# Optimization experiments

Measured on AMD Instinct MI355X. Metric: run time of the kernel, lower is better.

The kernel has to match this reference:

```python
import jax, jax.numpy as jnp
import numpy as np

N_NODES = 100000
N_EDGES = 1_600_000


def setup_inputs() -> dict:
    key = jax.random.key(0)
    ks = jax.random.split(key, 18)
    glorot = lambda k, fi, fo: jax.random.normal(k, (fi, fo), jnp.float32) * np.sqrt(2.0 / (fi + fo))
    inp = {
        "x": jax.random.normal(ks[0], (N_NODES, 5), jnp.float32),
        "edge_index": jax.random.randint(ks[1], (2, N_EDGES), 0, N_NODES, jnp.int64 if jax.config.jax_enable_x64 else jnp.int32),
        "W1": glorot(ks[2], 5, 32),  "b1": jnp.zeros((32,), jnp.float32),
        "W2": glorot(ks[3], 32, 32), "b2": jnp.zeros((32,), jnp.float32),
        "W3": glorot(ks[4], 32, 32), "b3": jnp.zeros((32,), jnp.float32),
        "Wd": glorot(ks[5], 32, 1),  "bd": jnp.zeros((1,), jnp.float32),
        "Wa": glorot(ks[6], 32, 1),  "ba": jnp.zeros((1,), jnp.float32),
        "Wt": glorot(ks[7], 32, 2),  "bt": jnp.zeros((2,), jnp.float32),
        "Wact": glorot(ks[8], 32, 9), "bact": jnp.zeros((9,), jnp.float32),
    }
    return inp


def _gcn_layer(x, row, col, norm, W, b):
    # GCNConv(add_self_loops=False): out[col] += norm * (x @ W)[row], then + bias
    h = x @ W                                  # [N, F_out]
    msg = h[row] * norm[:, None]               # [E, F_out]
    return jax.ops.segment_sum(msg, col, num_segments=N_NODES) + b


def reference(x, edge_index, W1, b1, W2, b2, W3, b3, Wd, bd, Wa, ba, Wt, bt, Wact, bact):
    row, col = edge_index[0], edge_index[1]
    # symmetric gcn normalization: deg over targets (unit edge weights)
    deg = jax.ops.segment_sum(jnp.ones((row.shape[0],), x.dtype), col, num_segments=N_NODES)
    dis = jnp.where(deg > 0, jax.lax.rsqrt(jnp.maximum(deg, 1.0)), 0.0)
    norm = dis[row] * dis[col]                 # [E]

    h = jax.nn.relu(_gcn_layer(x, row, col, norm, W1, b1))   # dropout = identity (eval)
    h = jax.nn.relu(_gcn_layer(h, row, col, norm, W2, b2))
    h = jax.nn.relu(_gcn_layer(h, row, col, norm, W3, b3))

    distance_scores = (h @ Wd + bd)[:, 0]      # [N]
    attention_scores = (h @ Wa + ba)[:, 0]     # [N]
    target_idx = jnp.argmax(attention_scores)
    h_t = h[target_idx]                        # [32]
    target_location_score = h_t @ Wt + bt      # [2]
    action_logits = h_t @ Wact + bact          # [9]
    return distance_scores, attention_scores, target_location_score, action_logits
```

## Files before the change

kernel.cpp:

```cpp
#include <hip/hip_runtime.h>
#include <hip/hip_fp16.h>
#include <math.h>


#define N_NODES 100000
#define F 32
#define BUCKET 64
#define NB ((N_NODES + BUCKET - 1) / BUCKET)
#define NBLK 256
#define SMAX 1536

__global__ void hist_kernel(const int* __restrict__ col, int* __restrict__ counts, int E) {
    __shared__ int hist[NB];
    int tid = threadIdx.x, blk = blockIdx.x;
    for (int i = tid; i < NB; i += 1024) hist[i] = 0;
    __syncthreads();
    int chunk = (((E + NBLK - 1) / NBLK) + 1) & ~1;
    int beg = blk * chunk;
    int end = beg + chunk; if (end > E) end = E;
    int cnt = end - beg; if (cnt < 0) cnt = 0;
    int pairs = cnt >> 1;
    const int2* c2 = (const int2*)(col + beg);
    for (int p = tid; p < pairs; p += 1024) {
        int2 v = c2[p];
        atomicAdd(&hist[v.x >> 6], 1);
        atomicAdd(&hist[v.y >> 6], 1);
    }
    if ((cnt & 1) && tid == 0) atomicAdd(&hist[col[end - 1] >> 6], 1);
    __syncthreads();
    for (int i = tid; i < NB; i += 1024) counts[(size_t)blk * NB + i] = hist[i];
}

__global__ void tot_kernel(const int* __restrict__ counts, int* __restrict__ tot) {
    int b = blockIdx.x * 256 + threadIdx.x;
    if (b >= NB) return;
    int s = 0;
    for (int blk = 0; blk < NBLK; blk++) s += counts[(size_t)blk * NB + b];
    tot[b] = s;
}

__global__ void offA_kernel(const int* __restrict__ tot, int* __restrict__ bucket_base,
                            int* __restrict__ rowstart) {
    __shared__ int psum[1024];
    int tid = threadIdx.x;
    int b0 = 2 * tid, b1 = 2 * tid + 1;
    int t0 = (b0 < NB) ? tot[b0] : 0;
    int t1 = (b1 < NB) ? tot[b1] : 0;
    int s = t0 + t1;
    psum[tid] = s;
    __syncthreads();
    for (int off = 1; off < 1024; off <<= 1) {
        int v = (tid >= off) ? psum[tid - off] : 0;
        __syncthreads();
        psum[tid] += v;
        __syncthreads();
    }
    int excl = psum[tid] - s;
    if (b0 < NB) bucket_base[b0] = excl;
    if (b1 < NB) bucket_base[b1] = excl + t0;
    if (tid == 1023) { bucket_base[NB] = psum[1023]; rowstart[N_NODES] = psum[1023]; }
}

__global__ void offB_kernel(const int* __restrict__ counts, const int* __restrict__ bucket_base,
                            int* __restrict__ boff) {
    int b = blockIdx.x * 256 + threadIdx.x;
    if (b >= NB) return;
    int running = bucket_base[b];
    for (int blk = 0; blk < NBLK; blk++) {
        boff[(size_t)blk * NB + b] = running;
        running += counts[(size_t)blk * NB + b];
    }
}

__global__ void scatter_kernel(const int* __restrict__ row, const int* __restrict__ col,
                               const int* __restrict__ boff, unsigned* __restrict__ storage, int E) {
    __shared__ int cur[NB];
    int tid = threadIdx.x, blk = blockIdx.x;
    for (int i = tid; i < NB; i += 1024) cur[i] = boff[(size_t)blk * NB + i];
    __syncthreads();
    int chunk = (((E + NBLK - 1) / NBLK) + 1) & ~1;
    int beg = blk * chunk;
    int end = beg + chunk; if (end > E) end = E;
    int cnt = end - beg; if (cnt < 0) cnt = 0;
    int pairs = cnt >> 1;
    const int2* c2 = (const int2*)(col + beg);
    const int2* r2 = (const int2*)(row + beg);
    for (int p = tid; p < pairs; p += 1024) {
        int2 c = c2[p];
        int2 r = r2[p];
        int pos0 = atomicAdd(&cur[c.x >> 6], 1);
        storage[pos0] = ((unsigned)(c.x & 63) << 17) | (unsigned)r.x;
        int pos1 = atomicAdd(&cur[c.y >> 6], 1);
        storage[pos1] = ((unsigned)(c.y & 63) << 17) | (unsigned)r.y;
    }
    if ((cnt & 1) && tid == 0) {
        int c = col[end - 1], r = row[end - 1];
        int pos = atomicAdd(&cur[c >> 6], 1);
        storage[pos] = ((unsigned)(c & 63) << 17) | (unsigned)r;
    }
}

__global__ void csr_build_kernel(const unsigned* __restrict__ storage, const int* __restrict__ bucket_base,
                                 int* __restrict__ rowstart, int* __restrict__ csr_src,
                                 float* __restrict__ dis, const float* __restrict__ x,
                                 float* __restrict__ xd, int n) {
    __shared__ unsigned sh[SMAX];
    __shared__ int outloc[SMAX];
    __shared__ int hist[BUCKET];
    __shared__ int pre[BUCKET];
    __shared__ int cur[BUCKET];
    __shared__ float dloc[BUCKET];
    int b = blockIdx.x, tid = threadIdx.x;
    if (tid < BUCKET) hist[tid] = 0;
    __syncthreads();
    int base = bucket_base[b];
    int tot = bucket_base[b + 1] - base;
    if (tot > SMAX) tot = SMAX;
    for (int i = tid; i < tot; i += 256) sh[i] = storage[base + i];
    __syncthreads();
    for (int i = tid; i < tot; i += 256) atomicAdd(&hist[sh[i] >> 17], 1);
    __syncthreads();
    if (tid < BUCKET) pre[tid] = hist[tid];
    __syncthreads();
    for (int off = 1; off < BUCKET; off <<= 1) {
        int v = 0;
        if (tid < BUCKET && tid >= off) v = pre[tid - off];
        __syncthreads();
        if (tid < BUCKET && tid >= off) pre[tid] += v;
        __syncthreads();
    }
    if (tid < BUCKET) {
        int excl = pre[tid] - hist[tid];
        cur[tid] = excl;
        int node = b * BUCKET + tid;
        if (node < n) {
            rowstart[node] = base + excl;
            int d = hist[tid];
            float dv = (d > 0) ? rsqrtf((float)d) : 0.0f;
            dis[node] = dv;
            dloc[tid] = dv;
        }
    }
    __syncthreads();
    for (int i = tid; i < BUCKET * 8; i += 256) {
        int nl = i >> 3, f = i & 7;
        int node = b * BUCKET + nl;
        if (node < n) xd[(size_t)node * 8 + f] = (f < 5) ? dloc[nl] * x[(size_t)node * 5 + f] : 0.0f;
    }
    for (int i = tid; i < tot; i += 256) {
        unsigned p = sh[i];
        int pos = atomicAdd(&cur[p >> 17], 1);
        outloc[pos] = (int)(p & 0x1FFFF);
    }
    __syncthreads();
    for (int i = tid; i < tot; i += 256) csr_src[base + i] = outloc[i];
}

__global__ void layer1_fused(const float* __restrict__ xd, const int* __restrict__ rowstart,
                             const int* __restrict__ csr_src, const float* __restrict__ dis,
                             const float* __restrict__ W1, const float* __restrict__ b1,
                             __half* __restrict__ gda, int n) {
    __shared__ float Ws[5 * F];
    __shared__ float s1s[32][8];
    int tid = threadIdx.x;
    if (tid < 5 * F) Ws[tid] = W1[tid];
    int grp = tid >> 3, f = tid & 7;
    int node = blockIdx.x * 32 + grp;
    float sum = 0.0f;
    if (node < n) {
        int start = rowstart[node], end = rowstart[node + 1];
        float a0 = 0, a1 = 0, a2 = 0, a3 = 0, a4 = 0, a5 = 0, a6 = 0, a7 = 0;
        int i = start;
        for (; i + 7 < end; i += 8) {
            int r0 = csr_src[i], r1 = csr_src[i+1], r2 = csr_src[i+2], r3 = csr_src[i+3];
            int r4 = csr_src[i+4], r5 = csr_src[i+5], r6 = csr_src[i+6], r7 = csr_src[i+7];
            a0 += xd[r0*8+f]; a1 += xd[r1*8+f]; a2 += xd[r2*8+f]; a3 += xd[r3*8+f];
            a4 += xd[r4*8+f]; a5 += xd[r5*8+f]; a6 += xd[r6*8+f]; a7 += xd[r7*8+f];
        }
        for (; i < end; i++) a0 += xd[csr_src[i]*8+f];
        sum = ((a0+a1)+(a2+a3)) + ((a4+a5)+(a6+a7));
    }
    s1s[grp][f] = sum;
    __syncthreads();
    if (node < n) {
        float dv = dis[node];
        float sk0 = dv * s1s[grp][0], sk1 = dv * s1s[grp][1], sk2 = dv * s1s[grp][2];
        float sk3 = dv * s1s[grp][3], sk4 = dv * s1s[grp][4];
        int fb = f * 4;
#pragma unroll
        for (int j = 0; j < 4; j++) {
            int ff = fb + j;
            float acc = b1[ff] + sk0 * Ws[0*F+ff] + sk1 * Ws[1*F+ff] + sk2 * Ws[2*F+ff]
                       + sk3 * Ws[3*F+ff] + sk4 * Ws[4*F+ff];
            float h = acc > 0.0f ? acc : 0.0f;
            gda[(size_t)node * F + ff] = __float2half(dv * h);
        }
    }
}

__device__ __forceinline__ void gather8lane(const uint2* __restrict__ gin2,
                                            const int* __restrict__ csr_src,
                                            int start, int end, int l, int E,
                                            float& a0, float& a1, float& a2, float& a3) {
    a0 = a1 = a2 = a3 = 0.0f;
    int i = start;
    if (i + 8 <= end) {
        int safe = i + l; if (safe > E - 1) safe = E - 1;
        int myidx = csr_src[safe];
        while (i + 8 <= end) {
            int nexti = i + 8;
            int nextidx = 0;
            if (nexti + 8 <= end) {
                int s2 = nexti + l; if (s2 > E - 1) s2 = E - 1;
                nextidx = csr_src[s2];
            }
#pragma unroll
            for (int j = 0; j < 8; j++) {
                int r = __shfl(myidx, j, 8);
                uint2 v = gin2[(size_t)r * 8 + l];
                __half2 h0 = *(__half2*)&v.x;
                __half2 h1 = *(__half2*)&v.y;
                float2 f0 = __half22float2(h0);
                float2 f1 = __half22float2(h1);
                a0 += f0.x; a1 += f0.y; a2 += f1.x; a3 += f1.y;
            }
            myidx = nextidx;
            i = nexti;
        }
    }
    for (; i < end; i++) {
        int r = csr_src[i];
        uint2 v = gin2[(size_t)r * 8 + l];
        __half2 h0 = *(__half2*)&v.x;
        __half2 h1 = *(__half2*)&v.y;
        float2 f0 = __half22float2(h0);
        float2 f1 = __half22float2(h1);
        a0 += f0.x; a1 += f0.y; a2 += f1.x; a3 += f1.y;
    }
}

__global__ void layer_mid_fused(const uint2* __restrict__ gin2, const int* __restrict__ rowstart,
                                const int* __restrict__ csr_src, const float* __restrict__ dis,
                                const float* __restrict__ W, const float* __restrict__ bb,
                                uint2* __restrict__ gout2, int n, int E) {
    __shared__ float Ws[F * F];
    __shared__ float hs[32][F + 1];
    int tid = threadIdx.x;
    for (int i = tid; i < F * F; i += 256) Ws[i] = W[i];
    int grp = tid >> 3;
    int l = tid & 7;
    int node = blockIdx.x * 32 + grp;
    int start = rowstart[node], end = rowstart[node + 1];
    float a0, a1, a2, a3;
    gather8lane(gin2, csr_src, start, end, l, E, a0, a1, a2, a3);
    float dv = dis[node];
    int fb = 4 * l;
    hs[grp][fb]     = dv * a0;
    hs[grp][fb + 1] = dv * a1;
    hs[grp][fb + 2] = dv * a2;
    hs[grp][fb + 3] = dv * a3;
    __syncthreads();
    float acc0 = bb[fb], acc1 = bb[fb+1], acc2 = bb[fb+2], acc3 = bb[fb+3];
#pragma unroll
    for (int k = 0; k < F; k++) {
        float hv = hs[grp][k];
        acc0 += hv * Ws[k*F+fb];
        acc1 += hv * Ws[k*F+fb+1];
        acc2 += hv * Ws[k*F+fb+2];
        acc3 += hv * Ws[k*F+fb+3];
    }
    float h0 = acc0 > 0.0f ? acc0 : 0.0f;
    float h1 = acc1 > 0.0f ? acc1 : 0.0f;
    float h2 = acc2 > 0.0f ? acc2 : 0.0f;
    float h3 = acc3 > 0.0f ? acc3 : 0.0f;
    __half2 o0 = __floats2half2_rn(dv * h0, dv * h1);
    __half2 o1 = __floats2half2_rn(dv * h2, dv * h3);
    uint2 pack;
    pack.x = *(unsigned*)&o0;
    pack.y = *(unsigned*)&o1;
    gout2[(size_t)node * 8 + l] = pack;
}

__global__ void layer_last_fused(const uint2* __restrict__ gin2, const int* __restrict__ rowstart,
                                 const int* __restrict__ csr_src, const float* __restrict__ dis,
                                 const float* __restrict__ W3, const float* __restrict__ b3,
                                 const float* __restrict__ Wd, const float* __restrict__ bd,
                                 const float* __restrict__ Wa, const float* __restrict__ ba,
                                 float* __restrict__ out, float* __restrict__ pmax,
                                 int* __restrict__ pidx, int n, int E) {
    __shared__ float Ws[F * F];
    __shared__ float hs[32][F + 1];
    __shared__ float gmax[32];
    __shared__ int gidx[32];
    int tid = threadIdx.x;
    for (int i = tid; i < F * F; i += 256) Ws[i] = W3[i];
    int grp = tid >> 3;
    int l = tid & 7;
    int node = blockIdx.x * 32 + grp;
    int start = rowstart[node], end = rowstart[node + 1];
    float a0, a1, a2, a3;
    gather8lane(gin2, csr_src, start, end, l, E, a0, a1, a2, a3);
    float dv = dis[node];
    int fb = 4 * l;
    hs[grp][fb]     = dv * a0;
    hs[grp][fb + 1] = dv * a1;
    hs[grp][fb + 2] = dv * a2;
    hs[grp][fb + 3] = dv * a3;
    __syncthreads();
    float acc0 = b3[fb], acc1 = b3[fb+1], acc2 = b3[fb+2], acc3 = b3[fb+3];
#pragma unroll
    for (int k = 0; k < F; k++) {
        float hv = hs[grp][k];
        acc0 += hv * Ws[k*F+fb];
        acc1 += hv * Ws[k*F+fb+1];
        acc2 += hv * Ws[k*F+fb+2];
        acc3 += hv * Ws[k*F+fb+3];
    }
    float h0 = acc0 > 0.0f ? acc0 : 0.0f;
    float h1 = acc1 > 0.0f ? acc1 : 0.0f;
    float h2 = acc2 > 0.0f ? acc2 : 0.0f;
    float h3 = acc3 > 0.0f ? acc3 : 0.0f;
    float dterm = h0 * Wd[fb] + h1 * Wd[fb+1] + h2 * Wd[fb+2] + h3 * Wd[fb+3];
    float aterm = h0 * Wa[fb] + h1 * Wa[fb+1] + h2 * Wa[fb+2] + h3 * Wa[fb+3];
#pragma unroll
    for (int off = 4; off > 0; off >>= 1) {
        dterm += __shfl_xor(dterm, off, 8);
        aterm += __shfl_xor(aterm, off, 8);
    }
    if (l == 0) {
        out[node] = dterm + bd[0];
        float asc = aterm + ba[0];
        out[N_NODES + node] = asc;
        gmax[grp] = asc;
        gidx[grp] = node;
    }
    __syncthreads();
    if (tid == 0) {
        float best = gmax[0]; int bi = gidx[0];
        for (int g = 1; g < 32; g++) {
            if (gmax[g] > best || (gmax[g] == best && gidx[g] < bi)) { best = gmax[g]; bi = gidx[g]; }
        }
        pmax[blockIdx.x] = best;
        pidx[blockIdx.x] = bi;
    }
}

__global__ void final_kernel(const float* __restrict__ pmax, const int* __restrict__ pidx, int nblocks,
                             const __half* __restrict__ gin, const int* __restrict__ rowstart,
                             const int* __restrict__ csr_src, const float* __restrict__ dis,
                             const float* __restrict__ W3, const float* __restrict__ b3,
                             const float* __restrict__ Wt, const float* __restrict__ bt,
                             const float* __restrict__ Wact, const float* __restrict__ bact,
                             float* __restrict__ out) {
    __shared__ float smax[256];
    __shared__ int sidx[256];
    __shared__ float part[8][F];
    __shared__ float hrow[F];
    __shared__ float ht[F];
    int tid = threadIdx.x;
    float best = -INFINITY; int bi = 0x7fffffff;
    for (int i = tid; i < nblocks; i += 256) {
        float v = pmax[i]; int ix = pidx[i];
        if (v > best || (v == best && ix < bi)) { best = v; bi = ix; }
    }
    smax[tid] = best; sidx[tid] = bi;
    __syncthreads();
    for (int st = 128; st > 0; st >>= 1) {
        if (tid < st) {
            float v2 = smax[tid + st]; int i2 = sidx[tid + st];
            if (v2 > smax[tid] || (v2 == smax[tid] && i2 < sidx[tid])) { smax[tid] = v2; sidx[tid] = i2; }
        }
        __syncthreads();
    }
    int target = sidx[0];
    int g = tid >> 5, f = tid & 31;
    int start = rowstart[target], end = rowstart[target + 1];
    float acc = 0.0f;
    for (int i = start + g; i < end; i += 8)
        acc += __half2float(gin[(size_t)csr_src[i] * F + f]);
    part[g][f] = acc;
    __syncthreads();
    if (tid < F) {
        float s = 0.0f;
#pragma unroll
        for (int gg = 0; gg < 8; gg++) s += part[gg][tid];
        hrow[tid] = dis[target] * s;
    }
    __syncthreads();
    if (tid < F) {
        float a = b3[tid];
#pragma unroll
        for (int k = 0; k < F; k++) a += hrow[k] * W3[k*F+tid];
        ht[tid] = a > 0.0f ? a : 0.0f;
    }
    __syncthreads();
    if (tid < 2) {
        float a = bt[tid];
#pragma unroll
        for (int k = 0; k < F; k++) a += ht[k] * Wt[k*2+tid];
        out[2 * N_NODES + tid] = a;
    } else if (tid < 11) {
        int j = tid - 2;
        float a = bact[j];
#pragma unroll
        for (int k = 0; k < F; k++) a += ht[k] * Wact[k*9+j];
        out[2 * N_NODES + 2 + j] = a;
    }
}

extern "C" void kernel_launch(void* const* d_in, const int* in_sizes, int n_in,
                              void* d_out, int out_size, void* d_ws, size_t ws_size,
                              hipStream_t stream) {
    const float* x  = (const float*)d_in[0];
    const int*   ei = (const int*)d_in[1];
    const int E = in_sizes[1] / 2;
    const int* row = ei;
    const int* col = ei + E;
    const float* W1 = (const float*)d_in[2];
    const float* b1 = (const float*)d_in[3];
    const float* W2 = (const float*)d_in[4];
    const float* b2 = (const float*)d_in[5];
    const float* W3 = (const float*)d_in[6];
    const float* b3 = (const float*)d_in[7];
    const float* Wd = (const float*)d_in[8];
    const float* bd = (const float*)d_in[9];
    const float* Wa = (const float*)d_in[10];
    const float* ba = (const float*)d_in[11];
    const float* Wt = (const float*)d_in[12];
    const float* bt = (const float*)d_in[13];
    const float* Wact = (const float*)d_in[14];
    const float* bact = (const float*)d_in[15];

    float* out = (float*)d_out;
    float* ws  = (float*)d_ws;

    float*    dis      = ws;
    float*    xd       = ws + N_NODES;
    __half*   gd_a     = (__half*)(ws + (size_t)17 * N_NODES);
    __half*   gd_b     = (__half*)(ws + (size_t)33 * N_NODES);
    unsigned* storage  = (unsigned*)(ws + (size_t)33 * N_NODES);
    int*      bucket_base = (int*)(ws + (size_t)49 * N_NODES);
    int*      counts   = bucket_base + NB + 1;
    int*      boff     = counts + NBLK * NB;
    int*      rowstart = boff + NBLK * NB;
    int*      csr_src  = rowstart + N_NODES + 1;
    float*    pmax     = (float*)(csr_src + E);
    int*      pidx     = (int*)(pmax + 12500);
    int*      tot      = pidx + 12500;

    const int B = 256;
    const int nb32 = (N_NODES + 31) / 32;

    hist_kernel<<<NBLK, 1024, 0, stream>>>(col, counts, E);
    tot_kernel<<<(NB + 255) / 256, B, 0, stream>>>(counts, tot);
    offA_kernel<<<1, 1024, 0, stream>>>(tot, bucket_base, rowstart);
    offB_kernel<<<(NB + 255) / 256, B, 0, stream>>>(counts, bucket_base, boff);
    scatter_kernel<<<NBLK, 1024, 0, stream>>>(row, col, boff, storage, E);
    csr_build_kernel<<<NB, B, 0, stream>>>(storage, bucket_base, rowstart, csr_src, dis, x, xd, N_NODES);

    layer1_fused<<<nb32, B, 0, stream>>>(xd, rowstart, csr_src, dis, W1, b1, gd_a, N_NODES);

    layer_mid_fused<<<nb32, B, 0, stream>>>((const uint2*)gd_a, rowstart, csr_src, dis,
                                            W2, b2, (uint2*)gd_b, N_NODES, E);

    layer_last_fused<<<nb32, B, 0, stream>>>((const uint2*)gd_b, rowstart, csr_src, dis,
                                             W3, b3, Wd, bd, Wa, ba, out, pmax, pidx, N_NODES, E);
    final_kernel<<<1, B, 0, stream>>>(pmax, pidx, nb32, gd_b, rowstart, csr_src, dis,
                                      W3, b3, Wt, bt, Wact, bact, out);
}
```

Before: 235.4 us.

## Merge bucket offset kernels into one wavefront-scan kernel with last-block finalization

Replaces the tot, offA and offB kernels with a single scan kernel. In it, each wavefront does an in-place exclusive scan of one bucket's per-block counts using shuffles, and the last block to arrive (found via an atomic ticket) scans the bucket totals into bucket_base. The scatter kernel then forms its offsets as the local prefix plus bucket_base, which removes the separate boff array. This saves two launches and the serial per-thread loops over 256 blocks, at the cost of threadfence and ticket synchronisation, and adds a ticket reset inside the hist kernel.

```diff
diff --git a/kernel.cpp b/kernel.cpp
--- a/kernel.cpp
+++ b/kernel.cpp
@@ -10,9 +10,11 @@
 #define NBLK 256
 #define SMAX 1536
 
-__global__ void hist_kernel(const int* __restrict__ col, int* __restrict__ counts, int E) {
+__global__ void hist_kernel(const int* __restrict__ col, int* __restrict__ counts, int E,
+                            int* __restrict__ ticket) {
     __shared__ int hist[NB];
     int tid = threadIdx.x, blk = blockIdx.x;
+    if (blk == 0 && tid == 0) *ticket = 0;
     for (int i = tid; i < NB; i += 1024) hist[i] = 0;
     __syncthreads();
     int chunk = (((E + NBLK - 1) / NBLK) + 1) & ~1;
@@ -31,52 +33,75 @@
     for (int i = tid; i < NB; i += 1024) counts[(size_t)blk * NB + i] = hist[i];
 }
 
-__global__ void tot_kernel(const int* __restrict__ counts, int* __restrict__ tot) {
-    int b = blockIdx.x * 256 + threadIdx.x;
-    if (b >= NB) return;
+__global__ void scan_kernel(int* __restrict__ counts, int* __restrict__ tot,
+                            int* __restrict__ bucket_base, int* __restrict__ rowstart,
+                            int* __restrict__ ticket) {
+    int tid = threadIdx.x;
+    int wid = tid >> 6, lane = tid & 63;
+    int b = blockIdx.x * 4 + wid;
+    if (b < NB) {
+        int run = 0;
+#pragma unroll
+        for (int k = 0; k < NBLK / 64; k++) {
+            int j = k * 64 + lane;
+            int v = counts[(size_t)j * NB + b];
+            int x = v;
+#pragma unroll
+            for (int off = 1; off < 64; off <<= 1) {
+                int y = __shfl_up(x, off, 64);
+                if (lane >= off) x += y;
+            }
+            counts[(size_t)j * NB + b] = run + (x - v);
+            run += __shfl(x, 63, 64);
+        }
+        if (lane == 0) tot[b] = run;
+    }
+    __shared__ int lastflag;
+    __threadfence();
+    __syncthreads();
+    if (tid == 0) lastflag = (atomicAdd(ticket, 1) == (int)gridDim.x - 1);
+    __syncthreads();
+    if (!lastflag) return;
+    __threadfence();
+    constexpr int PER = (NB + 255) / 256;
+    __shared__ int bsum[256];
+    int base = tid * PER;
+    int loc[PER];
     int s = 0;
-    for (int blk = 0; blk < NBLK; blk++) s += counts[(size_t)blk * NB + b];
-    tot[b] = s;
-}
-
-__global__ void offA_kernel(const int* __restrict__ tot, int* __restrict__ bucket_base,
-                            int* __restrict__ rowstart) {
-    __shared__ int psum[1024];
-    int tid = threadIdx.x;
-    int b0 = 2 * tid, b1 = 2 * tid + 1;
-    int t0 = (b0 < NB) ? tot[b0] : 0;
-    int t1 = (b1 < NB) ? tot[b1] : 0;
-    int s = t0 + t1;
-    psum[tid] = s;
-    __syncthreads();
-    for (int off = 1; off < 1024; off <<= 1) {
-        int v = (tid >= off) ? psum[tid - off] : 0;
+#pragma unroll
+    for (int k = 0; k < PER; k++) {
+        int idx = base + k;
+        int v = (idx < NB) ? tot[idx] : 0;
+        loc[k] = s;
+        s += v;
+    }
+    bsum[tid] = s;
+    __syncthreads();
+    for (int off = 1; off < 256; off <<= 1) {
+        int v = (tid >= off) ? bsum[tid - off] : 0;
         __syncthreads();
-        psum[tid] += v;
+        bsum[tid] += v;
         __syncthreads();
     }
-    int excl = psum[tid] - s;
-    if (b0 < NB) bucket_base[b0] = excl;
-    if (b1 < NB) bucket_base[b1] = excl + t0;
-    if (tid == 1023) { bucket_base[NB] = psum[1023]; rowstart[N_NODES] = psum[1023]; }
-}
-
-__global__ void offB_kernel(const int* __restrict__ counts, const int* __restrict__ bucket_base,
-                            int* __restrict__ boff) {
-    int b = blockIdx.x * 256 + threadIdx.x;
-    if (b >= NB) return;
-    int running = bucket_base[b];
-    for (int blk = 0; blk < NBLK; blk++) {
-        boff[(size_t)blk * NB + b] = running;
-        running += counts[(size_t)blk * NB + b];
+    int excl = bsum[tid] - s;
+#pragma unroll
+    for (int k = 0; k < PER; k++) {
+        int idx = base + k;
+        if (idx < NB) bucket_base[idx] = excl + loc[k];
+    }
+    if (tid == 255) {
+        bucket_base[NB] = bsum[255];
+        rowstart[N_NODES] = bsum[255];
     }
 }
 
 __global__ void scatter_kernel(const int* __restrict__ row, const int* __restrict__ col,
-                               const int* __restrict__ boff, unsigned* __restrict__ storage, int E) {
+                               const int* __restrict__ counts, const int* __restrict__ bucket_base,
+                               unsigned* __restrict__ storage, int E) {
     __shared__ int cur[NB];
     int tid = threadIdx.x, blk = blockIdx.x;
-    for (int i = tid; i < NB; i += 1024) cur[i] = boff[(size_t)blk * NB + i];
+    for (int i = tid; i < NB; i += 1024)
+        cur[i] = counts[(size_t)blk * NB + i] + bucket_base[i];
     __syncthreads();
     int chunk = (((E + NBLK - 1) / NBLK) + 1) & ~1;
     int beg = blk * chunk;
@@ -441,21 +466,19 @@
     unsigned* storage  = (unsigned*)(ws + (size_t)33 * N_NODES);
     int*      bucket_base = (int*)(ws + (size_t)49 * N_NODES);
     int*      counts   = bucket_base + NB + 1;
-    int*      boff     = counts + NBLK * NB;
-    int*      rowstart = boff + NBLK * NB;
+    int*      rowstart = counts + NBLK * NB;
     int*      csr_src  = rowstart + N_NODES + 1;
     float*    pmax     = (float*)(csr_src + E);
     int*      pidx     = (int*)(pmax + 12500);
     int*      tot      = pidx + 12500;
+    int*      ticket   = tot + NB;
 
     const int B = 256;
     const int nb32 = (N_NODES + 31) / 32;
 
-    hist_kernel<<<NBLK, 1024, 0, stream>>>(col, counts, E);
-    tot_kernel<<<(NB + 255) / 256, B, 0, stream>>>(counts, tot);
-    offA_kernel<<<1, 1024, 0, stream>>>(tot, bucket_base, rowstart);
-    offB_kernel<<<(NB + 255) / 256, B, 0, stream>>>(counts, bucket_base, boff);
-    scatter_kernel<<<NBLK, 1024, 0, stream>>>(row, col, boff, storage, E);
+    hist_kernel<<<NBLK, 1024, 0, stream>>>(col, counts, E, ticket);
+    scan_kernel<<<(NB + 3) / 4, B, 0, stream>>>(counts, tot, bucket_base, rowstart, ticket);
+    scatter_kernel<<<NBLK, 1024, 0, stream>>>(row, col, counts, bucket_base, storage, E);
     csr_build_kernel<<<NB, B, 0, stream>>>(storage, bucket_base, rowstart, csr_src, dis, x, xd, N_NODES);
 
     layer1_fused<<<nb32, B, 0, stream>>>(xd, rowstart, csr_src, dis, W1, b1, gd_a, N_NODES);
```

Measured after the change: 280.5 us. 19.1% more time.
